# Performance work log

Hardware: AMD Instinct MI355X
Metric: run time of the kernel (lower is better)

Reference implementation:

```python
import jax, jax.numpy as jnp
import numpy as np

B, S, F = 2, 2048, 1024
H, D = 16, 64
INIT = 0.02


def setup_inputs() -> dict:
    key = jax.random.key(0)
    k1, k2, k3 = jax.random.split(key, 3)
    x = jax.random.normal(k1, (B, S, F), dtype=jnp.float32)
    w_attn = jax.random.normal(k2, (F, 3 * F), dtype=jnp.float32) * INIT
    b_attn = jnp.zeros((3 * F,), dtype=jnp.float32)
    w_proj = jax.random.normal(k3, (F, F), dtype=jnp.float32) * INIT
    b_proj = jnp.zeros((F,), dtype=jnp.float32)
    return {"x": x, "w_attn": w_attn, "b_attn": b_attn, "w_proj": w_proj, "b_proj": b_proj}


def reference(x, w_attn, b_attn, w_proj, b_proj):
    # c_attn: [..., S, F] -> [..., S, 3F]
    qkv = jnp.einsum('bsf,fe->bse', x, w_attn) + b_attn
    q, k, v = jnp.split(qkv, 3, axis=-1)
    # split heads: [..., S, F] -> [..., S, H, D]
    q = q.reshape(q.shape[:-1] + (H, D))
    k = k.reshape(k.shape[:-1] + (H, D))
    v = v.reshape(v.shape[:-1] + (H, D))
    q = q / jnp.sqrt(jnp.asarray(D, dtype=q.dtype))
    # scores: [..., H, Sq, Sk]
    scores = jnp.einsum('bqhd,bkhd->bhqk', q, k)
    seq = x.shape[-2]
    causal = jnp.tril(jnp.ones((seq, seq), dtype=bool))  # [Sq, Sk]
    big_neg = jnp.finfo(scores.dtype).min
    scores = jnp.where(causal, scores, big_neg)
    weights = jax.nn.softmax(scores, axis=-1)
    z = jnp.einsum('bhqk,bkhd->bqhd', weights, v)
    merged = z.reshape(z.shape[:-2] + (F,))
    out = jnp.einsum('bsf,fe->bse', merged, w_proj) + b_proj
    return out
```

## Files before the change

kernel.cpp:

```cpp
#include <hip/hip_runtime.h>

#define B_ 2
#define S_ 2048
#define F_ 1024
#define H_ 16
#define D_ 64

typedef __bf16 bf16x8 __attribute__((ext_vector_type(8)));
typedef float f32x4 __attribute__((ext_vector_type(4)));
typedef float f32x16 __attribute__((ext_vector_type(16)));

union U8 { unsigned int u[4]; bf16x8 v; };

__device__ __forceinline__ unsigned short f2bf(float f) {
    union { float f; unsigned int u; } v;
    v.f = f;
    unsigned int r = v.u + 0x7fffu + ((v.u >> 16) & 1u);
    return (unsigned short)(r >> 16);
}

__device__ __forceinline__ unsigned int cvtpk_bf16(float lo, float hi) {
    unsigned int r;
    asm("v_cvt_pk_bf16_f32 %0, %1, %2" : "=v"(r) : "v"(lo), "v"(hi));
    return r;
}

__device__ __forceinline__ float xhalf_max(float x) {
    return fmaxf(x, __shfl_xor(x, 32));
}
__device__ __forceinline__ float xhalf_sum(float x) {
    return x + __shfl_xor(x, 32);
}

__device__ __forceinline__ void gload16(const unsigned short* g, unsigned short* l) {
    __builtin_amdgcn_global_load_lds(
        (const __attribute__((address_space(1))) unsigned int*)g,
        (__attribute__((address_space(3))) unsigned int*)l,
        16, 0, 0);
}

__global__ void cvt_kernel(const float* __restrict__ in, unsigned short* __restrict__ out, int n4) {
    int i = blockIdx.x * blockDim.x + threadIdx.x;
    if (i >= n4) return;
    float4 v = reinterpret_cast<const float4*>(in)[i];
    ushort4 o;
    o.x = f2bf(v.x); o.y = f2bf(v.y); o.z = f2bf(v.z); o.w = f2bf(v.w);
    reinterpret_cast<ushort4*>(out)[i] = o;
}

__global__ void tcvt_kernel(const float* __restrict__ in, unsigned short* __restrict__ out, int R, int C) {
    __shared__ float t[32][33];
    int r0 = blockIdx.y << 5, c0 = blockIdx.x << 5;
    int tx = threadIdx.x, ty = threadIdx.y;
#pragma unroll
    for (int kk = 0; kk < 4; ++kk)
        t[ty + 8 * kk][tx] = in[(size_t)(r0 + ty + 8 * kk) * C + c0 + tx];
    __syncthreads();
#pragma unroll
    for (int kk = 0; kk < 4; ++kk)
        out[(size_t)(c0 + ty + 8 * kk) * R + r0 + tx] = f2bf(t[tx][ty + 8 * kk]);
}

__global__ __launch_bounds__(256) void gemm_qkv(const unsigned short* __restrict__ A,
                                                const unsigned short* __restrict__ Bt,
                                                const float* __restrict__ bias,
                                                unsigned short* __restrict__ qo,
                                                unsigned short* __restrict__ ko,
                                                unsigned short* __restrict__ vo) {
    __shared__ __align__(16) unsigned short As[2 * 128 * 32];
    __shared__ __align__(16) unsigned short Bs[2 * 128 * 32];
    const int K = 1024, NT = 32;
    int m0 = blockIdx.y << 7, n0 = blockIdx.x << 7;
    int tid = threadIdx.x;
    int w = tid >> 6, l = tid & 63, lg = l >> 4, lr = l & 15;
    int wm = (w >> 1) << 6, wn = (w & 1) << 6;
    f32x4 acc[4][4] = {};

    int sr = tid >> 2, sc = (tid & 3) << 3;
    const unsigned short* Ab = A + (size_t)(m0 + sr) * K + sc;
    const unsigned short* Bb = Bt + (size_t)(n0 + sr) * K + sc;
    const size_t half = (size_t)64 * K;

    gload16(Ab, &As[tid * 8]);
    gload16(Ab + half, &As[2048 + tid * 8]);
    gload16(Bb, &Bs[tid * 8]);
    gload16(Bb + half, &Bs[2048 + tid * 8]);
    __syncthreads();

    for (int t = 0; t < NT; ++t) {
        int cur = (t & 1) * 4096;
        if (t + 1 < NT) {
            int nxt = ((t + 1) & 1) * 4096;
            int ko2 = (t + 1) * 32;
            gload16(Ab + ko2, &As[nxt + tid * 8]);
            gload16(Ab + ko2 + half, &As[nxt + 2048 + tid * 8]);
            gload16(Bb + ko2, &Bs[nxt + tid * 8]);
            gload16(Bb + ko2 + half, &Bs[nxt + 2048 + tid * 8]);
        }
        bf16x8 af[4], bfr[4];
#pragma unroll
        for (int mi = 0; mi < 4; ++mi)
            af[mi] = *reinterpret_cast<const bf16x8*>(&As[cur + (wm + mi * 16 + lr) * 32 + (lg << 3)]);
#pragma unroll
        for (int ni = 0; ni < 4; ++ni)
            bfr[ni] = *reinterpret_cast<const bf16x8*>(&Bs[cur + (wn + ni * 16 + lr) * 32 + (lg << 3)]);
#pragma unroll
        for (int mi = 0; mi < 4; ++mi)
#pragma unroll
            for (int ni = 0; ni < 4; ++ni)
                acc[mi][ni] = __builtin_amdgcn_mfma_f32_16x16x32_bf16(af[mi], bfr[ni], acc[mi][ni], 0, 0, 0);
        __syncthreads();
    }
#pragma unroll
    for (int mi = 0; mi < 4; ++mi) {
#pragma unroll
        for (int ni = 0; ni < 4; ++ni) {
            int col = n0 + wn + ni * 16 + lr;
            float bv = bias[col];
            int part = col >> 10, cc = col & 1023, h = cc >> 6, d = cc & 63;
            int row0 = m0 + wm + mi * 16 + (lg << 2);
            int bb = row0 >> 11, s0 = row0 & 2047;
            int bh = bb * H_ + h;
            if (part == 2) {
                int jt = s0 >> 5, db = d >> 5, kf2 = (s0 >> 4) & 1, hi2 = (s0 >> 3) & 1;
                int ll = (d & 31) | (hi2 << 5), e0 = s0 & 7;
                ushort4 pk;
                unsigned short* p = reinterpret_cast<unsigned short*>(&pk);
#pragma unroll
                for (int r = 0; r < 4; ++r) p[r] = f2bf(acc[mi][ni][r] + bv);
                *reinterpret_cast<ushort4*>(
                    &vo[(size_t)((((bh * 64 + jt) * 2 + db) * 2 + kf2)) * 512 + ll * 8 + e0]) = pk;
            } else {
                unsigned short* dst = part == 0 ? qo : ko;
                float scale = part == 0 ? 0.125f * 1.44269504f : 1.0f;
                int t2 = s0 >> 5, kf2 = d >> 4, e = d & 7;
                int lbase = ((d >> 3) & 1) << 5;
                size_t fb = (size_t)((bh * 64 + t2) * 4 + kf2) * 512 + e;
#pragma unroll
                for (int r = 0; r < 4; ++r) {
                    float vv = (acc[mi][ni][r] + bv) * scale;
                    dst[fb + (size_t)((((s0 + r) & 31) | lbase)) * 8] = f2bf(vv);
                }
            }
        }
    }
}

__global__ __launch_bounds__(256) void gemm_proj(const unsigned short* __restrict__ A,
                                                 const unsigned short* __restrict__ Bt,
                                                 const float* __restrict__ bias,
                                                 float* __restrict__ out) {
    __shared__ __align__(16) unsigned short As[2 * 128 * 32];
    __shared__ __align__(16) unsigned short Bs[2 * 128 * 32];
    const int K = 1024, NT = 32;
    int m0 = blockIdx.y << 7, n0 = blockIdx.x << 7;
    int tid = threadIdx.x;
    int w = tid >> 6, l = tid & 63, lg = l >> 4, lr = l & 15;
    int wm = (w >> 1) << 6, wn = (w & 1) << 6;
    f32x4 acc[4][4] = {};

    int sr = tid >> 2, sc = (tid & 3) << 3;
    const unsigned short* Ab = A + (size_t)(m0 + sr) * K + sc;
    const unsigned short* Bb = Bt + (size_t)(n0 + sr) * K + sc;
    const size_t half = (size_t)64 * K;

    gload16(Ab, &As[tid * 8]);
    gload16(Ab + half, &As[2048 + tid * 8]);
    gload16(Bb, &Bs[tid * 8]);
    gload16(Bb + half, &Bs[2048 + tid * 8]);
    __syncthreads();

    for (int t = 0; t < NT; ++t) {
        int cur = (t & 1) * 4096;
        if (t + 1 < NT) {
            int nxt = ((t + 1) & 1) * 4096;
            int ko2 = (t + 1) * 32;
            gload16(Ab + ko2, &As[nxt + tid * 8]);
            gload16(Ab + ko2 + half, &As[nxt + 2048 + tid * 8]);
            gload16(Bb + ko2, &Bs[nxt + tid * 8]);
            gload16(Bb + ko2 + half, &Bs[nxt + 2048 + tid * 8]);
        }
        bf16x8 af[4], bfr[4];
#pragma unroll
        for (int mi = 0; mi < 4; ++mi)
            af[mi] = *reinterpret_cast<const bf16x8*>(&As[cur + (wm + mi * 16 + lr) * 32 + (lg << 3)]);
#pragma unroll
        for (int ni = 0; ni < 4; ++ni)
            bfr[ni] = *reinterpret_cast<const bf16x8*>(&Bs[cur + (wn + ni * 16 + lr) * 32 + (lg << 3)]);
#pragma unroll
        for (int mi = 0; mi < 4; ++mi)
#pragma unroll
            for (int ni = 0; ni < 4; ++ni)
                acc[mi][ni] = __builtin_amdgcn_mfma_f32_16x16x32_bf16(af[mi], bfr[ni], acc[mi][ni], 0, 0, 0);
        __syncthreads();
    }
#pragma unroll
    for (int mi = 0; mi < 4; ++mi) {
#pragma unroll
        for (int ni = 0; ni < 4; ++ni) {
            int col = n0 + wn + ni * 16 + lr;
            float bv = bias[col];
#pragma unroll
            for (int r = 0; r < 4; ++r) {
                int row = m0 + wm + mi * 16 + (lg << 2) + r;
                out[(size_t)row * F_ + col] = acc[mi][ni][r] + bv;
            }
        }
    }
}

__device__ __forceinline__ void attn_tile32(
    const unsigned short* __restrict__ k, const unsigned short* __restrict__ v,
    int bh, int jt, bool pref, bool diag, int qcol, int hi, size_t lofs,
    const bf16x8 (&qf)[4], bf16x8 (&kcur)[4], bf16x8 (&knxt)[4],
    float &m, float &lsum, f32x16 &ot0, f32x16 &ot1)
{
    bf16x8 vf[4];
    const unsigned short* vp = v + (size_t)(bh * 64 + jt) * 2048 + lofs;
#pragma unroll
    for (int i = 0; i < 4; ++i)
        vf[i] = *reinterpret_cast<const bf16x8*>(vp + i * 512);
    if (pref) {
        const unsigned short* kp = k + (size_t)(bh * 64 + jt + 1) * 2048 + lofs;
#pragma unroll
        for (int kf = 0; kf < 4; ++kf)
            knxt[kf] = *reinterpret_cast<const bf16x8*>(kp + kf * 512);
    }

    f32x16 st = {};
#pragma unroll
    for (int kf = 0; kf < 4; ++kf)
        st = __builtin_amdgcn_mfma_f32_32x32x16_bf16(kcur[kf], qf[kf], st, 0, 0, 0);

    if (diag) {
        int qmh = qcol - 4 * hi;
#pragma unroll
        for (int r = 0; r < 16; ++r) {
            const int kbase = (r & 3) + 8 * (r >> 2);
            st[r] = (kbase > qmh) ? -1e30f : st[r];
        }
    }

    float pm = st[0];
#pragma unroll
    for (int r = 1; r < 16; ++r) pm = fmaxf(pm, st[r]);
    pm = xhalf_max(pm);

    if (!__all(pm <= m + 8.0f)) {
        float mn = fmaxf(m, pm);
        float scl = exp2f(m - mn);
        m = mn;
        lsum *= scl;
        ot0 *= scl;
        ot1 *= scl;
    }

    float ps = 0.f;
#pragma unroll
    for (int r = 0; r < 16; ++r) { st[r] = exp2f(st[r] - m); ps += st[r]; }
    lsum += ps;

    U8 pa0, pa1;
#pragma unroll
    for (int f = 0; f < 2; ++f) {
        unsigned int a0 = cvtpk_bf16(st[f * 8 + 0], st[f * 8 + 1]);
        unsigned int b0 = cvtpk_bf16(st[f * 8 + 4], st[f * 8 + 5]);
        asm("v_permlane32_swap_b32 %0, %1" : "+v"(a0), "+v"(b0));
        unsigned int a1 = cvtpk_bf16(st[f * 8 + 2], st[f * 8 + 3]);
        unsigned int b1 = cvtpk_bf16(st[f * 8 + 6], st[f * 8 + 7]);
        asm("v_permlane32_swap_b32 %0, %1" : "+v"(a1), "+v"(b1));
        U8& pa = f ? pa1 : pa0;
        pa.u[0] = a0; pa.u[1] = a1; pa.u[2] = b0; pa.u[3] = b1;
    }

    ot0 = __builtin_amdgcn_mfma_f32_32x32x16_bf16(vf[0], pa0.v, ot0, 0, 0, 0);
    ot0 = __builtin_amdgcn_mfma_f32_32x32x16_bf16(vf[1], pa1.v, ot0, 0, 0, 0);
    ot1 = __builtin_amdgcn_mfma_f32_32x32x16_bf16(vf[2], pa0.v, ot1, 0, 0, 0);
    ot1 = __builtin_amdgcn_mfma_f32_32x32x16_bf16(vf[3], pa1.v, ot1, 0, 0, 0);
}

__global__ __launch_bounds__(128, 3) void attn_kernel(const unsigned short* __restrict__ q,
                                                      const unsigned short* __restrict__ k,
                                                      const unsigned short* __restrict__ v,
                                                      unsigned short* __restrict__ z) {
    __shared__ __align__(16) float mbuf[64][36];
    int bh = blockIdx.x;
    int qt = gridDim.y - 1 - blockIdx.y;
    int q0 = qt << 5;
    int tid = threadIdx.x, w = tid >> 6, l = tid & 63;
    int qcol = l & 31, hi = l >> 5;
    size_t lofs = (size_t)l * 8;

    bf16x8 qf[4];
    {
        const unsigned short* qp = q + (size_t)(bh * 64 + qt) * 2048 + lofs;
#pragma unroll
        for (int kf = 0; kf < 4; ++kf)
            qf[kf] = *reinterpret_cast<const bf16x8*>(qp + kf * 512);
    }

    f32x16 ot0 = {}, ot1 = {};
    float m = -1e30f, lsum = 0.f;

    int ntk = qt + 1;
    int half = ntk >> 1;
    int start = w ? half : 0;
    int end = w ? ntk : half;

    if (start < end) {
        bf16x8 kA[4], kB[4];
        const unsigned short* kp = k + (size_t)(bh * 64 + start) * 2048 + lofs;
#pragma unroll
        for (int kf = 0; kf < 4; ++kf)
            kA[kf] = *reinterpret_cast<const bf16x8*>(kp + kf * 512);

        int jt = start;
        for (;;) {
            attn_tile32(k, v, bh, jt, jt + 1 < end, jt == qt, qcol, hi, lofs,
                        qf, kA, kB, m, lsum, ot0, ot1);
            if (++jt >= end) break;
            attn_tile32(k, v, bh, jt, jt + 1 < end, jt == qt, qcol, hi, lofs,
                        qf, kB, kA, m, lsum, ot0, ot1);
            if (++jt >= end) break;
        }
    }

    lsum = xhalf_sum(lsum);

    if (w == 1) {
        float* row = mbuf[l];
        row[0] = m;
        row[1] = lsum;
        *reinterpret_cast<f32x16*>(&row[4]) = ot0;
        *reinterpret_cast<f32x16*>(&row[20]) = ot1;
    }
    __syncthreads();
    if (w == 0) {
        float m1 = mbuf[l][0], l1 = mbuf[l][1];
        float mm = fmaxf(m, m1);
        float s0 = exp2f(m - mm), s1 = exp2f(m1 - mm);
        float lt = lsum * s0 + l1 * s1;
        f32x16 t0 = *reinterpret_cast<const f32x16*>(&mbuf[l][4]);
        f32x16 t1 = *reinterpret_cast<const f32x16*>(&mbuf[l][20]);
        ot0 = ot0 * s0 + t0 * s1;
        ot1 = ot1 * s0 + t1 * s1;

        float inv = 1.0f / lt;
        int b = bh >> 4, h = bh & 15;
        size_t zrow = ((size_t)(b * S_ + q0 + qcol)) * F_ + h * D_;
#pragma unroll
        for (int db = 0; db < 2; ++db) {
#pragma unroll
            for (int rq = 0; rq < 4; ++rq) {
                ushort4 pk;
                unsigned short* pp = reinterpret_cast<unsigned short*>(&pk);
#pragma unroll
                for (int i = 0; i < 4; ++i) {
                    float val = (db == 0 ? ot0[rq * 4 + i] : ot1[rq * 4 + i]) * inv;
                    pp[i] = f2bf(val);
                }
                *reinterpret_cast<ushort4*>(&z[zrow + db * 32 + rq * 8 + hi * 4]) = pk;
            }
        }
    }
}

extern "C" void kernel_launch(void* const* d_in, const int* in_sizes, int n_in,
                              void* d_out, int out_size, void* d_ws, size_t ws_size,
                              hipStream_t stream) {
    const float* x      = (const float*)d_in[0];
    const float* w_attn = (const float*)d_in[1];
    const float* b_attn = (const float*)d_in[2];
    const float* w_proj = (const float*)d_in[3];
    const float* b_proj = (const float*)d_in[4];
    float* out = (float*)d_out;
    char* ws = (char*)d_ws;

    unsigned short* xb   = (unsigned short*)(ws);
    unsigned short* wa_t = (unsigned short*)(ws + 8388608);
    unsigned short* wp_t = (unsigned short*)(ws + 14680064);
    unsigned short* qb   = (unsigned short*)(ws + 16777216);
    unsigned short* kb   = (unsigned short*)(ws + 25165824);
    unsigned short* vb   = (unsigned short*)(ws + 33554432);
    unsigned short* zb   = xb;

    cvt_kernel<<<4096, 256, 0, stream>>>(x, xb, (4096 * 1024) / 4);
    tcvt_kernel<<<dim3(96, 32), dim3(32, 8), 0, stream>>>(w_attn, wa_t, 1024, 3072);
    tcvt_kernel<<<dim3(32, 32), dim3(32, 8), 0, stream>>>(w_proj, wp_t, 1024, 1024);
    gemm_qkv<<<dim3(24, 32), 256, 0, stream>>>(xb, wa_t, b_attn, qb, kb, vb);
    attn_kernel<<<dim3(32, 64), 128, 0, stream>>>(qb, kb, vb, zb);
    gemm_proj<<<dim3(8, 32), 256, 0, stream>>>(zb, wp_t, b_proj, out);
}
```

Measured before the change: 122.7 us.

## Split attention KV range across four waves per block with LDS merge

Each attention block now runs four waves instead of two, and each wave processes a quarter of the causal key tiles. The partial softmax states (max, sum, output accumulators) of waves 1-3 go to LDS and wave 0 merges them before writing Z. This targets the serial key loop per query tile and aims to shorten latency-bound blocks. In exchange it uses more LDS per block, adds more merge work, and leaves short query tiles with idle waves.

```diff
diff --git a/kernel.cpp b/kernel.cpp
--- a/kernel.cpp
+++ b/kernel.cpp
@@ -279,11 +279,11 @@
     ot1 = __builtin_amdgcn_mfma_f32_32x32x16_bf16(vf[3], pa1.v, ot1, 0, 0, 0);
 }
 
-__global__ __launch_bounds__(128, 3) void attn_kernel(const unsigned short* __restrict__ q,
+__global__ __launch_bounds__(256, 3) void attn_kernel(const unsigned short* __restrict__ q,
                                                       const unsigned short* __restrict__ k,
                                                       const unsigned short* __restrict__ v,
                                                       unsigned short* __restrict__ z) {
-    __shared__ __align__(16) float mbuf[64][36];
+    __shared__ __align__(16) float mbuf[3][64][36];
     int bh = blockIdx.x;
     int qt = gridDim.y - 1 - blockIdx.y;
     int q0 = qt << 5;
@@ -303,11 +303,12 @@
     float m = -1e30f, lsum = 0.f;
 
     int ntk = qt + 1;
-    int half = ntk >> 1;
-    int start = w ? half : 0;
-    int end = w ? ntk : half;
-
-    if (start < end) {
+    int bs = ntk >> 2, rem = ntk & 3;
+    int cnt = bs + ((w >= 4 - rem) ? 1 : 0);
+    int start = bs * w + ((w - (4 - rem)) > 0 ? (w - (4 - rem)) : 0);
+    int end = start + cnt;
+
+    if (cnt > 0) {
         bf16x8 kA[4], kB[4];
         const unsigned short* kp = k + (size_t)(bh * 64 + start) * 2048 + lofs;
 #pragma unroll
@@ -327,8 +328,8 @@
 
     lsum = xhalf_sum(lsum);
 
-    if (w == 1) {
-        float* row = mbuf[l];
+    if (w) {
+        float* row = mbuf[w - 1][l];
         row[0] = m;
         row[1] = lsum;
         *reinterpret_cast<f32x16*>(&row[4]) = ot0;
@@ -336,16 +337,21 @@
     }
     __syncthreads();
     if (w == 0) {
-        float m1 = mbuf[l][0], l1 = mbuf[l][1];
-        float mm = fmaxf(m, m1);
-        float s0 = exp2f(m - mm), s1 = exp2f(m1 - mm);
-        float lt = lsum * s0 + l1 * s1;
-        f32x16 t0 = *reinterpret_cast<const f32x16*>(&mbuf[l][4]);
-        f32x16 t1 = *reinterpret_cast<const f32x16*>(&mbuf[l][20]);
-        ot0 = ot0 * s0 + t0 * s1;
-        ot1 = ot1 * s0 + t1 * s1;
-
-        float inv = 1.0f / lt;
+        float mw0 = mbuf[0][l][0], mw1 = mbuf[1][l][0], mw2 = mbuf[2][l][0];
+        float mm = fmaxf(fmaxf(m, mw0), fmaxf(mw1, mw2));
+        float s0 = exp2f(m - mm);
+        lsum *= s0; ot0 *= s0; ot1 *= s0;
+#pragma unroll
+        for (int i = 0; i < 3; ++i) {
+            float sw = exp2f(mbuf[i][l][0] - mm);
+            lsum += mbuf[i][l][1] * sw;
+            f32x16 t0 = *reinterpret_cast<const f32x16*>(&mbuf[i][l][4]);
+            f32x16 t1 = *reinterpret_cast<const f32x16*>(&mbuf[i][l][20]);
+            ot0 += t0 * sw;
+            ot1 += t1 * sw;
+        }
+
+        float inv = 1.0f / lsum;
         int b = bh >> 4, h = bh & 15;
         size_t zrow = ((size_t)(b * S_ + q0 + qcol)) * F_ + h * D_;
 #pragma unroll
@@ -388,6 +394,6 @@
     tcvt_kernel<<<dim3(96, 32), dim3(32, 8), 0, stream>>>(w_attn, wa_t, 1024, 3072);
     tcvt_kernel<<<dim3(32, 32), dim3(32, 8), 0, stream>>>(w_proj, wp_t, 1024, 1024);
     gemm_qkv<<<dim3(24, 32), 256, 0, stream>>>(xb, wa_t, b_attn, qb, kb, vb);
-    attn_kernel<<<dim3(32, 64), 128, 0, stream>>>(qb, kb, vb, zb);
+    attn_kernel<<<dim3(32, 64), 256, 0, stream>>>(qb, kb, vb, zb);
     gemm_proj<<<dim3(8, 32), 256, 0, stream>>>(zb, wp_t, b_proj, out);
 }
```

New measurement: 121.3 us. No clear change (-1.2%).

## Share double-buffered K/V tiles in LDS across four query-tile waves

Applied to the files above, without the earlier changes.

The attention kernel now runs 4 waves per block, each owning one 32-row query tile, instead of 2 waves splitting the key range of one query tile. K/V tiles are loaded once per block into double-buffered shared memory with gload16 and read by all waves. This cuts redundant global K/V traffic and removes the cross-wave softmax merge. In exchange it adds a block-wide barrier per key tile, and waves with earlier query tiles sit idle for the last tiles, so causal load imbalance inside a block grows.

```diff
diff --git a/kernel.cpp b/kernel.cpp
--- a/kernel.cpp
+++ b/kernel.cpp
@@ -209,28 +209,18 @@
     }
 }
 
-__device__ __forceinline__ void attn_tile32(
-    const unsigned short* __restrict__ k, const unsigned short* __restrict__ v,
-    int bh, int jt, bool pref, bool diag, int qcol, int hi, size_t lofs,
-    const bf16x8 (&qf)[4], bf16x8 (&kcur)[4], bf16x8 (&knxt)[4],
+__device__ __forceinline__ void attn_tile_lds(
+    const unsigned short* Kt, const unsigned short* Vt,
+    bool diag, int qcol, int hi, int lofs,
+    const bf16x8 (&qf)[4],
     float &m, float &lsum, f32x16 &ot0, f32x16 &ot1)
 {
-    bf16x8 vf[4];
-    const unsigned short* vp = v + (size_t)(bh * 64 + jt) * 2048 + lofs;
-#pragma unroll
-    for (int i = 0; i < 4; ++i)
-        vf[i] = *reinterpret_cast<const bf16x8*>(vp + i * 512);
-    if (pref) {
-        const unsigned short* kp = k + (size_t)(bh * 64 + jt + 1) * 2048 + lofs;
-#pragma unroll
-        for (int kf = 0; kf < 4; ++kf)
-            knxt[kf] = *reinterpret_cast<const bf16x8*>(kp + kf * 512);
-    }
-
     f32x16 st = {};
 #pragma unroll
-    for (int kf = 0; kf < 4; ++kf)
-        st = __builtin_amdgcn_mfma_f32_32x32x16_bf16(kcur[kf], qf[kf], st, 0, 0, 0);
+    for (int kf = 0; kf < 4; ++kf) {
+        bf16x8 kf8 = *reinterpret_cast<const bf16x8*>(&Kt[kf * 512 + lofs]);
+        st = __builtin_amdgcn_mfma_f32_32x32x16_bf16(kf8, qf[kf], st, 0, 0, 0);
+    }
 
     if (diag) {
         int qmh = qcol - 4 * hi;
@@ -273,23 +263,29 @@
         pa.u[0] = a0; pa.u[1] = a1; pa.u[2] = b0; pa.u[3] = b1;
     }
 
-    ot0 = __builtin_amdgcn_mfma_f32_32x32x16_bf16(vf[0], pa0.v, ot0, 0, 0, 0);
-    ot0 = __builtin_amdgcn_mfma_f32_32x32x16_bf16(vf[1], pa1.v, ot0, 0, 0, 0);
-    ot1 = __builtin_amdgcn_mfma_f32_32x32x16_bf16(vf[2], pa0.v, ot1, 0, 0, 0);
-    ot1 = __builtin_amdgcn_mfma_f32_32x32x16_bf16(vf[3], pa1.v, ot1, 0, 0, 0);
-}
-
-__global__ __launch_bounds__(128, 3) void attn_kernel(const unsigned short* __restrict__ q,
-                                                      const unsigned short* __restrict__ k,
-                                                      const unsigned short* __restrict__ v,
-                                                      unsigned short* __restrict__ z) {
-    __shared__ __align__(16) float mbuf[64][36];
+    bf16x8 vf0 = *reinterpret_cast<const bf16x8*>(&Vt[0 * 512 + lofs]);
+    bf16x8 vf1 = *reinterpret_cast<const bf16x8*>(&Vt[1 * 512 + lofs]);
+    bf16x8 vf2 = *reinterpret_cast<const bf16x8*>(&Vt[2 * 512 + lofs]);
+    bf16x8 vf3 = *reinterpret_cast<const bf16x8*>(&Vt[3 * 512 + lofs]);
+    ot0 = __builtin_amdgcn_mfma_f32_32x32x16_bf16(vf0, pa0.v, ot0, 0, 0, 0);
+    ot0 = __builtin_amdgcn_mfma_f32_32x32x16_bf16(vf1, pa1.v, ot0, 0, 0, 0);
+    ot1 = __builtin_amdgcn_mfma_f32_32x32x16_bf16(vf2, pa0.v, ot1, 0, 0, 0);
+    ot1 = __builtin_amdgcn_mfma_f32_32x32x16_bf16(vf3, pa1.v, ot1, 0, 0, 0);
+}
+
+__global__ __launch_bounds__(256) void attn_kernel(const unsigned short* __restrict__ q,
+                                                   const unsigned short* __restrict__ k,
+                                                   const unsigned short* __restrict__ v,
+                                                   unsigned short* __restrict__ z) {
+    __shared__ __align__(16) unsigned short Ks[2][2048];
+    __shared__ __align__(16) unsigned short Vs[2][2048];
     int bh = blockIdx.x;
-    int qt = gridDim.y - 1 - blockIdx.y;
-    int q0 = qt << 5;
+    int qg = gridDim.y - 1 - blockIdx.y;
     int tid = threadIdx.x, w = tid >> 6, l = tid & 63;
     int qcol = l & 31, hi = l >> 5;
-    size_t lofs = (size_t)l * 8;
+    int lofs = l * 8;
+    int qt = 4 * qg + w;
+    int maxjt = 4 * qg + 3;
 
     bf16x8 qf[4];
     {
@@ -302,65 +298,43 @@
     f32x16 ot0 = {}, ot1 = {};
     float m = -1e30f, lsum = 0.f;
 
-    int ntk = qt + 1;
-    int half = ntk >> 1;
-    int start = w ? half : 0;
-    int end = w ? ntk : half;
-
-    if (start < end) {
-        bf16x8 kA[4], kB[4];
-        const unsigned short* kp = k + (size_t)(bh * 64 + start) * 2048 + lofs;
-#pragma unroll
-        for (int kf = 0; kf < 4; ++kf)
-            kA[kf] = *reinterpret_cast<const bf16x8*>(kp + kf * 512);
-
-        int jt = start;
-        for (;;) {
-            attn_tile32(k, v, bh, jt, jt + 1 < end, jt == qt, qcol, hi, lofs,
-                        qf, kA, kB, m, lsum, ot0, ot1);
-            if (++jt >= end) break;
-            attn_tile32(k, v, bh, jt, jt + 1 < end, jt == qt, qcol, hi, lofs,
-                        qf, kB, kA, m, lsum, ot0, ot1);
-            if (++jt >= end) break;
-        }
+    const unsigned short* kb = k + (size_t)(bh * 64) * 2048;
+    const unsigned short* vb = v + (size_t)(bh * 64) * 2048;
+
+    gload16(kb + tid * 8, &Ks[0][tid * 8]);
+    gload16(vb + tid * 8, &Vs[0][tid * 8]);
+    __syncthreads();
+
+    for (int jt = 0; jt <= maxjt; ++jt) {
+        int cur = jt & 1;
+        if (jt < maxjt) {
+            int nxt = cur ^ 1;
+            gload16(kb + (size_t)(jt + 1) * 2048 + tid * 8, &Ks[nxt][tid * 8]);
+            gload16(vb + (size_t)(jt + 1) * 2048 + tid * 8, &Vs[nxt][tid * 8]);
+        }
+        if (jt <= qt)
+            attn_tile_lds(Ks[cur], Vs[cur], jt == qt, qcol, hi, lofs,
+                          qf, m, lsum, ot0, ot1);
+        __syncthreads();
     }
 
     lsum = xhalf_sum(lsum);
 
-    if (w == 1) {
-        float* row = mbuf[l];
-        row[0] = m;
-        row[1] = lsum;
-        *reinterpret_cast<f32x16*>(&row[4]) = ot0;
-        *reinterpret_cast<f32x16*>(&row[20]) = ot1;
-    }
-    __syncthreads();
-    if (w == 0) {
-        float m1 = mbuf[l][0], l1 = mbuf[l][1];
-        float mm = fmaxf(m, m1);
-        float s0 = exp2f(m - mm), s1 = exp2f(m1 - mm);
-        float lt = lsum * s0 + l1 * s1;
-        f32x16 t0 = *reinterpret_cast<const f32x16*>(&mbuf[l][4]);
-        f32x16 t1 = *reinterpret_cast<const f32x16*>(&mbuf[l][20]);
-        ot0 = ot0 * s0 + t0 * s1;
-        ot1 = ot1 * s0 + t1 * s1;
-
-        float inv = 1.0f / lt;
-        int b = bh >> 4, h = bh & 15;
-        size_t zrow = ((size_t)(b * S_ + q0 + qcol)) * F_ + h * D_;
-#pragma unroll
-        for (int db = 0; db < 2; ++db) {
-#pragma unroll
-            for (int rq = 0; rq < 4; ++rq) {
-                ushort4 pk;
-                unsigned short* pp = reinterpret_cast<unsigned short*>(&pk);
-#pragma unroll
-                for (int i = 0; i < 4; ++i) {
-                    float val = (db == 0 ? ot0[rq * 4 + i] : ot1[rq * 4 + i]) * inv;
-                    pp[i] = f2bf(val);
-                }
-                *reinterpret_cast<ushort4*>(&z[zrow + db * 32 + rq * 8 + hi * 4]) = pk;
+    float inv = 1.0f / lsum;
+    int b = bh >> 4, h = bh & 15;
+    size_t zrow = ((size_t)(b * S_ + qt * 32 + qcol)) * F_ + h * D_;
+#pragma unroll
+    for (int db = 0; db < 2; ++db) {
+#pragma unroll
+        for (int rq = 0; rq < 4; ++rq) {
+            ushort4 pk;
+            unsigned short* pp = reinterpret_cast<unsigned short*>(&pk);
+#pragma unroll
+            for (int i = 0; i < 4; ++i) {
+                float val = (db == 0 ? ot0[rq * 4 + i] : ot1[rq * 4 + i]) * inv;
+                pp[i] = f2bf(val);
             }
+            *reinterpret_cast<ushort4*>(&z[zrow + db * 32 + rq * 8 + hi * 4]) = pk;
         }
     }
 }
@@ -388,6 +362,6 @@
     tcvt_kernel<<<dim3(96, 32), dim3(32, 8), 0, stream>>>(w_attn, wa_t, 1024, 3072);
     tcvt_kernel<<<dim3(32, 32), dim3(32, 8), 0, stream>>>(w_proj, wp_t, 1024, 1024);
     gemm_qkv<<<dim3(24, 32), 256, 0, stream>>>(xb, wa_t, b_attn, qb, kb, vb);
-    attn_kernel<<<dim3(32, 64), 128, 0, stream>>>(qb, kb, vb, zb);
+    attn_kernel<<<dim3(32, 16), 256, 0, stream>>>(qb, kb, vb, zb);
     gemm_proj<<<dim3(8, 32), 256, 0, stream>>>(zb, wp_t, b_proj, out);
 }
```

Measured after the change: 154.9 us. +26.2%, slower.
